# Optimization experiments

Measured on AMD Instinct MI355X. Metric: run time of the kernel, lower is better.

Reference implementation:

```python
import jax, jax.numpy as jnp
import numpy as np

K = 3
K2 = K * K
EPS = 1e-5


def conv2d(x, w, stride=1, pad=1):
    return jax.lax.conv_general_dilated(
        x, w, (stride, stride), [(pad, pad), (pad, pad)],
        dimension_numbers=("NCHW", "OIHW", "NCHW"))


def bilinear_sample(x, py, px):
    """x: [B,C,H,W]; py,px: [B,Ho,Wo,K2] float sample coords.
    Zero padding outside bounds (torchvision deform_conv2d semantics).
    Returns [B,C,Ho,Wo,K2]."""
    B, C, H, W = x.shape
    Ho, Wo = py.shape[1], py.shape[2]
    y0 = jnp.floor(py)
    x0 = jnp.floor(px)
    wy1 = py - y0
    wx1 = px - x0
    x_flat = x.reshape(B, C, H * W)

    def gather(yi, xi):
        valid = (yi >= 0) & (yi < H) & (xi >= 0) & (xi < W)
        yc = jnp.clip(yi, 0, H - 1).astype(jnp.int32)
        xc = jnp.clip(xi, 0, W - 1).astype(jnp.int32)
        idx = (yc * W + xc).reshape(B, 1, -1)          # [B,1,N]
        v = jnp.take_along_axis(x_flat, idx, axis=2)   # [B,C,N]
        return v * valid.reshape(B, 1, -1).astype(x.dtype)

    w00 = ((1 - wy1) * (1 - wx1)).reshape(B, 1, -1)
    w01 = ((1 - wy1) * wx1).reshape(B, 1, -1)
    w10 = (wy1 * (1 - wx1)).reshape(B, 1, -1)
    w11 = (wy1 * wx1).reshape(B, 1, -1)
    val = (w00 * gather(y0, x0) + w01 * gather(y0, x0 + 1)
           + w10 * gather(y0 + 1, x0) + w11 * gather(y0 + 1, x0 + 1))
    return val.reshape(B, C, Ho, Wo, K2)


def deform_conv_bn_relu(x, d, offset_w, conv_w, gamma, beta):
    # offset branch: 3x3 conv on d, clamp to [-1,1]
    offset = jnp.clip(conv2d(d, offset_w, 1, 1), -1.0, 1.0)  # [B,2*K2,H,W]
    B, Cin, H, W = x.shape
    Cout = conv_w.shape[0]
    off = offset.reshape(B, K2, 2, H, W)
    dy = off[:, :, 0].transpose(0, 2, 3, 1)  # [B,H,W,K2]
    dx = off[:, :, 1].transpose(0, 2, 3, 1)
    kh = (jnp.arange(K2) // K).astype(jnp.float32)
    kw = (jnp.arange(K2) % K).astype(jnp.float32)
    # sample coords: out pixel + kernel tap - padding + learned offset
    py = (jnp.arange(H, dtype=jnp.float32)[None, :, None, None] - 1.0
          + kh[None, None, None, :] + dy)
    px = (jnp.arange(W, dtype=jnp.float32)[None, None, :, None] - 1.0
          + kw[None, None, None, :] + dx)
    sampled = bilinear_sample(x, py, px)  # [B,Cin,H,W,K2]
    out = jnp.einsum('bchwk,ock->bohw', sampled,
                     conv_w.reshape(Cout, Cin, K2))
    # BatchNorm2d (training forward: biased batch stats) + ReLU
    mean = out.mean(axis=(0, 2, 3))
    var = out.var(axis=(0, 2, 3))
    inv = gamma / jnp.sqrt(var + EPS)
    out = (out - mean[None, :, None, None]) * inv[None, :, None, None] \
        + beta[None, :, None, None]
    out = jax.nn.relu(out)
    return out, offset


def setup_inputs() -> dict:
    key = jax.random.key(0)
    k1, k2, k3, k4 = jax.random.split(key, 4)
    B, C, H, W = 4, 64, 160, 160
    Cout, offC = 64, 64
    x = jax.random.normal(k1, (B, C, H, W), dtype=jnp.float32)
    d = jax.random.normal(k2, (B, offC, H, W), dtype=jnp.float32)
    # torch zero-inits offset_conv; use small random weights so the
    # bilinear gather path is actually exercised with fractional offsets
    offset_w = jax.random.normal(k3, (2 * K2, offC, K, K), dtype=jnp.float32) * 0.01
    conv_w = jax.random.normal(k4, (Cout, C, K, K), dtype=jnp.float32) * (1.0 / np.sqrt(C * K2))
    gamma = jnp.ones((Cout,), dtype=jnp.float32)
    beta = jnp.zeros((Cout,), dtype=jnp.float32)
    return {"x": x, "d": d, "offset_w": offset_w, "conv_w": conv_w,
            "gamma": gamma, "beta": beta}


def reference(x, d, offset_w, conv_w, gamma, beta):
    return deform_conv_bn_relu(x, d, offset_w, conv_w, gamma, beta)
```

## Files before the change

kernel.cpp:

```cpp
#include <hip/hip_runtime.h>
#include <hip/hip_bf16.h>

#define BB 4
#define HH 160
#define WW 160
#define HWD (HH * WW)
#define OUT_ELEMS (BB * 64 * HWD)
#define OFF_ELEMS (BB * 18 * HWD)
#define EPSBN 1e-5f
#define CHSTRIDE (8 * HWD)
#define NSLOT 256

typedef __attribute__((ext_vector_type(8))) short bf16x8;
typedef __attribute__((ext_vector_type(4))) float f32x4;

__device__ inline unsigned pack2bf(float a, float b) {
  __hip_bfloat162 h2 = __float22bfloat162_rn(float2{a, b});
  unsigned u;
  __builtin_memcpy(&u, &h2, 4);
  return u;
}
__device__ inline unsigned short bf16bits(float a) {
  __hip_bfloat16 h = __float2bfloat16(a);
  unsigned short u;
  __builtin_memcpy(&u, &h, 2);
  return u;
}

__device__ inline void tile_map(int blk, int& b, int& ty0, int& tx0) {
  int t = (blk & 7) * 200 + (blk >> 3);
  b = t / 400;
  int r = t % 400;
  ty0 = (r / 10) * 4;
  tx0 = (r % 10) * 16;
}

__global__ void prep_kernel(const float* __restrict__ cw,
                            const float* __restrict__ ow,
                            unsigned short* __restrict__ Bp,
                            unsigned short* __restrict__ B2p,
                            float* __restrict__ part) {
  int i = blockIdx.x * 256 + threadIdx.x;
  if (i < 32768) part[i] = 0.f;
  if (i < 49152) {
    int j = i & 7, l = (i >> 3) & 63, rest = i >> 9;
    int ki = rest % 24, nt = rest / 24;
    int kp = ki * 32 + ((l >> 4) << 3) + j;
    int chunk = kp / 96, kq = kp % 96;
    int t = kq >> 3, c = kq & 7;
    int n = nt * 16 + (l & 15);
    float v = (t < 9) ? cw[n * 576 + (chunk * 8 + c) * 9 + t] : 0.f;
    Bp[i] = bf16bits(v);
  }
  if (i < 24576) {
    int j = i & 7, l = (i >> 3) & 63, rest = i >> 9;
    int ki = rest % 24, nt = rest / 24;
    int kp = ki * 32 + ((l >> 4) << 3) + j;
    int chunk = kp / 96, kq = kp % 96;
    int t = kq >> 3, c = kq & 7;
    int n = nt * 16 + (l & 15);
    float v = (t < 9 && n < 18) ? ow[n * 576 + (chunk * 8 + c) * 9 + t] : 0.f;
    B2p[i] = bf16bits(v);
  }
}

__global__ __launch_bounds__(256) void offconv_kernel(
    const float* __restrict__ d, const bf16x8* __restrict__ B2p,
    float* __restrict__ off_out) {
  int b, ty0, tx0;
  tile_map(blockIdx.x, b, ty0, tx0);
  const int tid = threadIdx.x;
  const int wv = tid >> 6, lane = tid & 63;
  const int lo = lane >> 4, li = lane & 15;
  const int px = li, py = wv;

  __shared__ float p2[108 * 12];
  __shared__ bf16x8 Af[768];

  int poff[3];
  bool tre[3];
#pragma unroll
  for (int kk = 0; kk < 3; ++kk) {
    int t = kk * 4 + lo;
    tre[kk] = (t < 9);
    poff[kk] = tre[kk] ? ((py + t / 3) * 18 + px + t % 3) : 0;
  }

  int goff[4], laddr[4];
  bool gok[4];
#pragma unroll
  for (int i = 0; i < 4; ++i) {
    int l = tid + i * 256;
    int c = l / 108, rc = l % 108, r = rc / 18, col = rc % 18;
    int gy = ty0 - 1 + r, gx = tx0 - 1 + col;
    gok[i] = (l < 864) && gy >= 0 && gy < HH && gx >= 0 && gx < WW;
    goff[i] = ((b * 64 + c) * HH + gy) * WW + gx;
    laddr[i] = rc * 12 + c;
  }
  float g[4];
#pragma unroll
  for (int i = 0; i < 4; ++i) g[i] = gok[i] ? d[goff[i]] : 0.f;

  f32x4 acc0{0.f, 0.f, 0.f, 0.f}, acc1{0.f, 0.f, 0.f, 0.f};
  const int nt = wv >> 1, mh = wv & 1;

  for (int chunk = 0; chunk < 8; ++chunk) {
    bf16x8 bw0 = B2p[((nt * 24 + chunk * 3 + 0) << 6) + lane];
    bf16x8 bw1 = B2p[((nt * 24 + chunk * 3 + 1) << 6) + lane];
    bf16x8 bw2 = B2p[((nt * 24 + chunk * 3 + 2) << 6) + lane];
#pragma unroll
    for (int i = 0; i < 4; ++i) {
      int l = tid + i * 256;
      if (l < 864) p2[laddr[i]] = g[i];
    }
    __syncthreads();
    int nco = ((chunk < 7) ? (chunk + 1) : 7) * CHSTRIDE;
#pragma unroll
    for (int i = 0; i < 4; ++i) g[i] = gok[i] ? d[goff[i] + nco] : 0.f;
#pragma unroll
    for (int kk = 0; kk < 3; ++kk) {
      union { bf16x8 v; unsigned u[4]; } a;
      if (tre[kk]) {
        const float* q = p2 + poff[kk] * 12;
        float4 c0 = *(const float4*)(q);
        float4 c1 = *(const float4*)(q + 4);
        a.u[0] = pack2bf(c0.x, c0.y);
        a.u[1] = pack2bf(c0.z, c0.w);
        a.u[2] = pack2bf(c1.x, c1.y);
        a.u[3] = pack2bf(c1.z, c1.w);
      } else {
        a.u[0] = a.u[1] = a.u[2] = a.u[3] = 0u;
      }
      Af[((wv * 3 + kk) << 6) + lane] = a.v;
    }
    __syncthreads();
#pragma unroll
    for (int kk = 0; kk < 3; ++kk) {
      bf16x8 bw = (kk == 0) ? bw0 : (kk == 1) ? bw1 : bw2;
      acc0 = __builtin_amdgcn_mfma_f32_16x16x32_bf16(
          Af[(((mh * 2) * 3 + kk) << 6) + lane], bw, acc0, 0, 0, 0);
      acc1 = __builtin_amdgcn_mfma_f32_16x16x32_bf16(
          Af[(((mh * 2 + 1) * 3 + kk) << 6) + lane], bw, acc1, 0, 0, 0);
    }
  }
  const int n = nt * 16 + li;
  if (n < 18) {
#pragma unroll
    for (int f = 0; f < 2; ++f) {
      int mf = mh * 2 + f;
      f32x4 a = f ? acc1 : acc0;
      float* po = off_out + ((b * 18 + n) * HH + ty0 + mf) * WW + tx0 + lo * 4;
      float4 v;
      v.x = fminf(1.f, fmaxf(-1.f, a[0]));
      v.y = fminf(1.f, fmaxf(-1.f, a[1]));
      v.z = fminf(1.f, fmaxf(-1.f, a[2]));
      v.w = fminf(1.f, fmaxf(-1.f, a[3]));
      *(float4*)po = v;
    }
  }
}

__global__ __launch_bounds__(256) void dconv_kernel(
    const float* __restrict__ x, const float* __restrict__ offs,
    const bf16x8* __restrict__ Bp, float* __restrict__ out,
    float* __restrict__ part) {
  int b, ty0, tx0;
  tile_map(blockIdx.x, b, ty0, tx0);
  const int tid = threadIdx.x;
  const int wv = tid >> 6, lane = tid & 63;
  const int lo = lane >> 4, li = lane & 15;
  const int px = li, py = wv;
  const int h = ty0 + py, w = tx0 + px;

  __shared__ float patch[189 * 12];
  __shared__ bf16x8 Af[768];

  int bs[3];
  float W00[3], W01[3], W10[3], W11[3];
  bool tre[3];
#pragma unroll
  for (int kk = 0; kk < 3; ++kk) {
    int t = kk * 4 + lo;
    tre[kk] = (t < 9);
    if (tre[kk]) {
      float dy = offs[((b * 18 + 2 * t) * HH + h) * WW + w];
      float dx = offs[((b * 18 + 2 * t + 1) * HH + h) * WW + w];
      float pyf = (float)(h - 1 + t / 3) + dy;
      float pxf = (float)(w - 1 + t % 3) + dx;
      float y0 = floorf(pyf), x0 = floorf(pxf);
      float wy = pyf - y0, wx = pxf - x0;
      bs[kk] = ((int)y0 - (ty0 - 2)) * 21 + ((int)x0 - (tx0 - 2));
      W00[kk] = (1.f - wy) * (1.f - wx);
      W01[kk] = (1.f - wy) * wx;
      W10[kk] = wy * (1.f - wx);
      W11[kk] = wy * wx;
    } else {
      bs[kk] = 0;
      W00[kk] = W01[kk] = W10[kk] = W11[kk] = 0.f;
    }
  }

  int goff[6], laddr[6];
  bool gok[6];
#pragma unroll
  for (int i = 0; i < 6; ++i) {
    int l = tid + i * 256;
    int c = l / 189, rc = l % 189, r = rc / 21, col = rc % 21;
    int gy = ty0 - 2 + r, gx = tx0 - 2 + col;
    gok[i] = (l < 1512) && gy >= 0 && gy < HH && gx >= 0 && gx < WW;
    goff[i] = ((b * 64 + c) * HH + gy) * WW + gx;
    laddr[i] = rc * 12 + c;
  }
  float g[6];
#pragma unroll
  for (int i = 0; i < 6; ++i) g[i] = gok[i] ? x[goff[i]] : 0.f;

  f32x4 acc[4];
#pragma unroll
  for (int i = 0; i < 4; ++i) acc[i] = f32x4{0.f, 0.f, 0.f, 0.f};
  const int nt = wv;

  for (int chunk = 0; chunk < 8; ++chunk) {
    bf16x8 bw0 = Bp[((nt * 24 + chunk * 3 + 0) << 6) + lane];
    bf16x8 bw1 = Bp[((nt * 24 + chunk * 3 + 1) << 6) + lane];
    bf16x8 bw2 = Bp[((nt * 24 + chunk * 3 + 2) << 6) + lane];
#pragma unroll
    for (int i = 0; i < 6; ++i) {
      int l = tid + i * 256;
      if (l < 1512) patch[laddr[i]] = g[i];
    }
    __syncthreads();
    int nco = ((chunk < 7) ? (chunk + 1) : 7) * CHSTRIDE;
#pragma unroll
    for (int i = 0; i < 6; ++i) g[i] = gok[i] ? x[goff[i] + nco] : 0.f;
#pragma unroll
    for (int kk = 0; kk < 3; ++kk) {
      union { bf16x8 v; unsigned u[4]; } a;
      if (tre[kk]) {
        const float* q = patch + bs[kk] * 12;
        float4 p00a = *(const float4*)(q);
        float4 p00b = *(const float4*)(q + 4);
        float4 p01a = *(const float4*)(q + 12);
        float4 p01b = *(const float4*)(q + 16);
        float4 p10a = *(const float4*)(q + 252);
        float4 p10b = *(const float4*)(q + 256);
        float4 p11a = *(const float4*)(q + 264);
        float4 p11b = *(const float4*)(q + 268);
        float w0 = W00[kk], w1 = W01[kk], w2 = W10[kk], w3 = W11[kk];
        float v0 = fmaf(w3, p11a.x, fmaf(w2, p10a.x, fmaf(w1, p01a.x, w0 * p00a.x)));
        float v1 = fmaf(w3, p11a.y, fmaf(w2, p10a.y, fmaf(w1, p01a.y, w0 * p00a.y)));
        float v2 = fmaf(w3, p11a.z, fmaf(w2, p10a.z, fmaf(w1, p01a.z, w0 * p00a.z)));
        float v3 = fmaf(w3, p11a.w, fmaf(w2, p10a.w, fmaf(w1, p01a.w, w0 * p00a.w)));
        float v4 = fmaf(w3, p11b.x, fmaf(w2, p10b.x, fmaf(w1, p01b.x, w0 * p00b.x)));
        float v5 = fmaf(w3, p11b.y, fmaf(w2, p10b.y, fmaf(w1, p01b.y, w0 * p00b.y)));
        float v6 = fmaf(w3, p11b.z, fmaf(w2, p10b.z, fmaf(w1, p01b.z, w0 * p00b.z)));
        float v7 = fmaf(w3, p11b.w, fmaf(w2, p10b.w, fmaf(w1, p01b.w, w0 * p00b.w)));
        a.u[0] = pack2bf(v0, v1);
        a.u[1] = pack2bf(v2, v3);
        a.u[2] = pack2bf(v4, v5);
        a.u[3] = pack2bf(v6, v7);
      } else {
        a.u[0] = a.u[1] = a.u[2] = a.u[3] = 0u;
      }
      Af[((wv * 3 + kk) << 6) + lane] = a.v;
    }
    __syncthreads();
#pragma unroll
    for (int kk = 0; kk < 3; ++kk) {
      bf16x8 bw = (kk == 0) ? bw0 : (kk == 1) ? bw1 : bw2;
#pragma unroll
      for (int mf = 0; mf < 4; ++mf)
        acc[mf] = __builtin_amdgcn_mfma_f32_16x16x32_bf16(
            Af[((mf * 3 + kk) << 6) + lane], bw, acc[mf], 0, 0, 0);
    }
  }
  const int n = nt * 16 + li;
  float s = 0.f, s2 = 0.f;
#pragma unroll
  for (int mf = 0; mf < 4; ++mf) {
    float* po = out + ((b * 64 + n) * HH + ty0 + mf) * WW + tx0 + lo * 4;
    *(float4*)po = make_float4(acc[mf][0], acc[mf][1], acc[mf][2], acc[mf][3]);
#pragma unroll
    for (int r = 0; r < 4; ++r) {
      float v = acc[mf][r];
      s += v;
      s2 = fmaf(v, v, s2);
    }
  }
  s += __shfl_xor(s, 16);  s += __shfl_xor(s, 32);
  s2 += __shfl_xor(s2, 16); s2 += __shfl_xor(s2, 32);
  if (lo == 0) {
    int slot = blockIdx.x & (NSLOT - 1);
    atomicAdd(&part[n * NSLOT + slot], s);
    atomicAdd(&part[(64 + n) * NSLOT + slot], s2);
  }
}

__global__ __launch_bounds__(256) void reduce_kernel(
    const float* __restrict__ part, double* __restrict__ sums) {
  const int j = blockIdx.x;
  __shared__ double sh[256];
  sh[threadIdx.x] = (double)part[j * NSLOT + threadIdx.x];
  __syncthreads();
  for (int t = 128; t > 0; t >>= 1) {
    if (threadIdx.x < t) sh[threadIdx.x] += sh[threadIdx.x + t];
    __syncthreads();
  }
  if (threadIdx.x == 0) sums[j] = sh[0];
}

__global__ __launch_bounds__(256) void bnapply_kernel(
    float* __restrict__ out, const double* __restrict__ sums,
    const float* __restrict__ gamma, const float* __restrict__ beta) {
  const int i = blockIdx.x * 256 + threadIdx.x;
  if (i >= OUT_ELEMS / 4) return;
  const int o = (i / (HWD / 4)) & 63;
  const float n_inv = 1.0f / (float)(BB * HWD);
  float mean = (float)sums[o] * n_inv;
  float var = (float)sums[64 + o] * n_inv - mean * mean;
  float inv = gamma[o] * rsqrtf(var + EPSBN);
  float bt = beta[o];
  float4 v = ((float4*)out)[i];
  v.x = fmaxf(0.f, (v.x - mean) * inv + bt);
  v.y = fmaxf(0.f, (v.y - mean) * inv + bt);
  v.z = fmaxf(0.f, (v.z - mean) * inv + bt);
  v.w = fmaxf(0.f, (v.w - mean) * inv + bt);
  ((float4*)out)[i] = v;
}

extern "C" void kernel_launch(void* const* d_in, const int* in_sizes, int n_in,
                              void* d_out, int out_size, void* d_ws, size_t ws_size,
                              hipStream_t stream) {
  const float* x = (const float*)d_in[0];
  const float* d = (const float*)d_in[1];
  const float* ow = (const float*)d_in[2];
  const float* cw = (const float*)d_in[3];
  const float* gamma = (const float*)d_in[4];
  const float* beta = (const float*)d_in[5];

  float* out = (float*)d_out;
  float* off_out = out + OUT_ELEMS;

  double* sums = (double*)d_ws;
  unsigned short* Bp = (unsigned short*)((char*)d_ws + 1024);
  unsigned short* B2p = Bp + 49152;
  float* part = (float*)(B2p + 24576);

  prep_kernel<<<192, 256, 0, stream>>>(cw, ow, Bp, B2p, part);

  offconv_kernel<<<1600, 256, 0, stream>>>(d, (const bf16x8*)B2p, off_out);
  dconv_kernel<<<1600, 256, 0, stream>>>(x, off_out, (const bf16x8*)Bp, out,
                                         part);

  reduce_kernel<<<128, 256, 0, stream>>>(part, sums);
  bnapply_kernel<<<(OUT_ELEMS / 4 + 255) / 256, 256, 0, stream>>>(
      out, sums, gamma, beta);
}
```

Baseline: 166.9 us.

## Fuse offset conv and deformable conv into one kernel via shared-memory offsets

Merges the offset-convolution kernel into the deformable-convolution kernel so each tile computes its clamped offsets, stores them in shared memory, and reads them back directly instead of round-tripping through global memory. One kernel launch goes away, and the first x-patch loads are issued before the offset write-out so they overlap with it. The fused kernel needs more shared memory and registers, and it adds launch_bounds(256,4), which can push the compiler into register spills or limit occupancy.

```diff
diff --git a/kernel.cpp b/kernel.cpp
--- a/kernel.cpp
+++ b/kernel.cpp
@@ -64,105 +64,10 @@
   }
 }
 
-__global__ __launch_bounds__(256) void offconv_kernel(
-    const float* __restrict__ d, const bf16x8* __restrict__ B2p,
-    float* __restrict__ off_out) {
-  int b, ty0, tx0;
-  tile_map(blockIdx.x, b, ty0, tx0);
-  const int tid = threadIdx.x;
-  const int wv = tid >> 6, lane = tid & 63;
-  const int lo = lane >> 4, li = lane & 15;
-  const int px = li, py = wv;
-
-  __shared__ float p2[108 * 12];
-  __shared__ bf16x8 Af[768];
-
-  int poff[3];
-  bool tre[3];
-#pragma unroll
-  for (int kk = 0; kk < 3; ++kk) {
-    int t = kk * 4 + lo;
-    tre[kk] = (t < 9);
-    poff[kk] = tre[kk] ? ((py + t / 3) * 18 + px + t % 3) : 0;
-  }
-
-  int goff[4], laddr[4];
-  bool gok[4];
-#pragma unroll
-  for (int i = 0; i < 4; ++i) {
-    int l = tid + i * 256;
-    int c = l / 108, rc = l % 108, r = rc / 18, col = rc % 18;
-    int gy = ty0 - 1 + r, gx = tx0 - 1 + col;
-    gok[i] = (l < 864) && gy >= 0 && gy < HH && gx >= 0 && gx < WW;
-    goff[i] = ((b * 64 + c) * HH + gy) * WW + gx;
-    laddr[i] = rc * 12 + c;
-  }
-  float g[4];
-#pragma unroll
-  for (int i = 0; i < 4; ++i) g[i] = gok[i] ? d[goff[i]] : 0.f;
-
-  f32x4 acc0{0.f, 0.f, 0.f, 0.f}, acc1{0.f, 0.f, 0.f, 0.f};
-  const int nt = wv >> 1, mh = wv & 1;
-
-  for (int chunk = 0; chunk < 8; ++chunk) {
-    bf16x8 bw0 = B2p[((nt * 24 + chunk * 3 + 0) << 6) + lane];
-    bf16x8 bw1 = B2p[((nt * 24 + chunk * 3 + 1) << 6) + lane];
-    bf16x8 bw2 = B2p[((nt * 24 + chunk * 3 + 2) << 6) + lane];
-#pragma unroll
-    for (int i = 0; i < 4; ++i) {
-      int l = tid + i * 256;
-      if (l < 864) p2[laddr[i]] = g[i];
-    }
-    __syncthreads();
-    int nco = ((chunk < 7) ? (chunk + 1) : 7) * CHSTRIDE;
-#pragma unroll
-    for (int i = 0; i < 4; ++i) g[i] = gok[i] ? d[goff[i] + nco] : 0.f;
-#pragma unroll
-    for (int kk = 0; kk < 3; ++kk) {
-      union { bf16x8 v; unsigned u[4]; } a;
-      if (tre[kk]) {
-        const float* q = p2 + poff[kk] * 12;
-        float4 c0 = *(const float4*)(q);
-        float4 c1 = *(const float4*)(q + 4);
-        a.u[0] = pack2bf(c0.x, c0.y);
-        a.u[1] = pack2bf(c0.z, c0.w);
-        a.u[2] = pack2bf(c1.x, c1.y);
-        a.u[3] = pack2bf(c1.z, c1.w);
-      } else {
-        a.u[0] = a.u[1] = a.u[2] = a.u[3] = 0u;
-      }
-      Af[((wv * 3 + kk) << 6) + lane] = a.v;
-    }
-    __syncthreads();
-#pragma unroll
-    for (int kk = 0; kk < 3; ++kk) {
-      bf16x8 bw = (kk == 0) ? bw0 : (kk == 1) ? bw1 : bw2;
-      acc0 = __builtin_amdgcn_mfma_f32_16x16x32_bf16(
-          Af[(((mh * 2) * 3 + kk) << 6) + lane], bw, acc0, 0, 0, 0);
-      acc1 = __builtin_amdgcn_mfma_f32_16x16x32_bf16(
-          Af[(((mh * 2 + 1) * 3 + kk) << 6) + lane], bw, acc1, 0, 0, 0);
-    }
-  }
-  const int n = nt * 16 + li;
-  if (n < 18) {
-#pragma unroll
-    for (int f = 0; f < 2; ++f) {
-      int mf = mh * 2 + f;
-      f32x4 a = f ? acc1 : acc0;
-      float* po = off_out + ((b * 18 + n) * HH + ty0 + mf) * WW + tx0 + lo * 4;
-      float4 v;
-      v.x = fminf(1.f, fmaxf(-1.f, a[0]));
-      v.y = fminf(1.f, fmaxf(-1.f, a[1]));
-      v.z = fminf(1.f, fmaxf(-1.f, a[2]));
-      v.w = fminf(1.f, fmaxf(-1.f, a[3]));
-      *(float4*)po = v;
-    }
-  }
-}
-
-__global__ __launch_bounds__(256) void dconv_kernel(
-    const float* __restrict__ x, const float* __restrict__ offs,
-    const bf16x8* __restrict__ Bp, float* __restrict__ out,
+__global__ __launch_bounds__(256, 4) void fused_kernel(
+    const float* __restrict__ x, const float* __restrict__ d,
+    const bf16x8* __restrict__ Bp, const bf16x8* __restrict__ B2p,
+    float* __restrict__ out, float* __restrict__ off_out,
     float* __restrict__ part) {
   int b, ty0, tx0;
   tile_map(blockIdx.x, b, ty0, tx0);
@@ -174,6 +79,116 @@
 
   __shared__ float patch[189 * 12];
   __shared__ bf16x8 Af[768];
+  __shared__ float offs_s[64 * 18];
+
+  int goffx[6], laddrx[6];
+  bool gokx[6];
+#pragma unroll
+  for (int i = 0; i < 6; ++i) {
+    int l = tid + i * 256;
+    int c = l / 189, rc = l % 189, r = rc / 21, col = rc % 21;
+    int gy = ty0 - 2 + r, gx = tx0 - 2 + col;
+    gokx[i] = (l < 1512) && gy >= 0 && gy < HH && gx >= 0 && gx < WW;
+    goffx[i] = ((b * 64 + c) * HH + gy) * WW + gx;
+    laddrx[i] = rc * 12 + c;
+  }
+
+  f32x4 acc0{0.f, 0.f, 0.f, 0.f}, acc1{0.f, 0.f, 0.f, 0.f};
+  const int ntA = wv >> 1, mh = wv & 1;
+  {
+    int poff[3];
+    bool tre[3];
+#pragma unroll
+    for (int kk = 0; kk < 3; ++kk) {
+      int t = kk * 4 + lo;
+      tre[kk] = (t < 9);
+      poff[kk] = tre[kk] ? ((py + t / 3) * 18 + px + t % 3) : 0;
+    }
+
+    int goff[4], laddr[4];
+    bool gok[4];
+#pragma unroll
+    for (int i = 0; i < 4; ++i) {
+      int l = tid + i * 256;
+      int c = l / 108, rc = l % 108, r = rc / 18, col = rc % 18;
+      int gy = ty0 - 1 + r, gx = tx0 - 1 + col;
+      gok[i] = (l < 864) && gy >= 0 && gy < HH && gx < WW && gx >= 0;
+      goff[i] = ((b * 64 + c) * HH + gy) * WW + gx;
+      laddr[i] = rc * 12 + c;
+    }
+    float g[4];
+#pragma unroll
+    for (int i = 0; i < 4; ++i) g[i] = gok[i] ? d[goff[i]] : 0.f;
+
+    for (int chunk = 0; chunk < 8; ++chunk) {
+      bf16x8 bw0 = B2p[((ntA * 24 + chunk * 3 + 0) << 6) + lane];
+      bf16x8 bw1 = B2p[((ntA * 24 + chunk * 3 + 1) << 6) + lane];
+      bf16x8 bw2 = B2p[((ntA * 24 + chunk * 3 + 2) << 6) + lane];
+#pragma unroll
+      for (int i = 0; i < 4; ++i) {
+        int l = tid + i * 256;
+        if (l < 864) patch[laddr[i]] = g[i];
+      }
+      __syncthreads();
+      int nco = ((chunk < 7) ? (chunk + 1) : 7) * CHSTRIDE;
+#pragma unroll
+      for (int i = 0; i < 4; ++i) g[i] = gok[i] ? d[goff[i] + nco] : 0.f;
+#pragma unroll
+      for (int kk = 0; kk < 3; ++kk) {
+        union { bf16x8 v; unsigned u[4]; } a;
+        if (tre[kk]) {
+          const float* q = patch + poff[kk] * 12;
+          float4 c0 = *(const float4*)(q);
+          float4 c1 = *(const float4*)(q + 4);
+          a.u[0] = pack2bf(c0.x, c0.y);
+          a.u[1] = pack2bf(c0.z, c0.w);
+          a.u[2] = pack2bf(c1.x, c1.y);
+          a.u[3] = pack2bf(c1.z, c1.w);
+        } else {
+          a.u[0] = a.u[1] = a.u[2] = a.u[3] = 0u;
+        }
+        Af[((wv * 3 + kk) << 6) + lane] = a.v;
+      }
+      __syncthreads();
+#pragma unroll
+      for (int kk = 0; kk < 3; ++kk) {
+        bf16x8 bw = (kk == 0) ? bw0 : (kk == 1) ? bw1 : bw2;
+        acc0 = __builtin_amdgcn_mfma_f32_16x16x32_bf16(
+            Af[(((mh * 2) * 3 + kk) << 6) + lane], bw, acc0, 0, 0, 0);
+        acc1 = __builtin_amdgcn_mfma_f32_16x16x32_bf16(
+            Af[(((mh * 2 + 1) * 3 + kk) << 6) + lane], bw, acc1, 0, 0, 0);
+      }
+    }
+  }
+
+  float gv[6];
+#pragma unroll
+  for (int i = 0; i < 6; ++i) gv[i] = gokx[i] ? x[goffx[i]] : 0.f;
+
+  {
+    const int n = ntA * 16 + li;
+    if (n < 18) {
+#pragma unroll
+      for (int f = 0; f < 2; ++f) {
+        int mf = mh * 2 + f;
+        f32x4 a = f ? acc1 : acc0;
+        float* po =
+            off_out + ((b * 18 + n) * HH + ty0 + mf) * WW + tx0 + lo * 4;
+        float4 v;
+        v.x = fminf(1.f, fmaxf(-1.f, a[0]));
+        v.y = fminf(1.f, fmaxf(-1.f, a[1]));
+        v.z = fminf(1.f, fmaxf(-1.f, a[2]));
+        v.w = fminf(1.f, fmaxf(-1.f, a[3]));
+        *(float4*)po = v;
+        int pix = mf * 16 + lo * 4;
+        offs_s[(pix + 0) * 18 + n] = v.x;
+        offs_s[(pix + 1) * 18 + n] = v.y;
+        offs_s[(pix + 2) * 18 + n] = v.z;
+        offs_s[(pix + 3) * 18 + n] = v.w;
+      }
+    }
+  }
+  __syncthreads();
 
   int bs[3];
   float W00[3], W01[3], W10[3], W11[3];
@@ -183,8 +198,8 @@
     int t = kk * 4 + lo;
     tre[kk] = (t < 9);
     if (tre[kk]) {
-      float dy = offs[((b * 18 + 2 * t) * HH + h) * WW + w];
-      float dx = offs[((b * 18 + 2 * t + 1) * HH + h) * WW + w];
+      float dy = offs_s[(py * 16 + px) * 18 + 2 * t];
+      float dx = offs_s[(py * 16 + px) * 18 + 2 * t + 1];
       float pyf = (float)(h - 1 + t / 3) + dy;
       float pxf = (float)(w - 1 + t % 3) + dx;
       float y0 = floorf(pyf), x0 = floorf(pxf);
@@ -200,21 +215,6 @@
     }
   }
 
-  int goff[6], laddr[6];
-  bool gok[6];
-#pragma unroll
-  for (int i = 0; i < 6; ++i) {
-    int l = tid + i * 256;
-    int c = l / 189, rc = l % 189, r = rc / 21, col = rc % 21;
-    int gy = ty0 - 2 + r, gx = tx0 - 2 + col;
-    gok[i] = (l < 1512) && gy >= 0 && gy < HH && gx >= 0 && gx < WW;
-    goff[i] = ((b * 64 + c) * HH + gy) * WW + gx;
-    laddr[i] = rc * 12 + c;
-  }
-  float g[6];
-#pragma unroll
-  for (int i = 0; i < 6; ++i) g[i] = gok[i] ? x[goff[i]] : 0.f;
-
   f32x4 acc[4];
 #pragma unroll
   for (int i = 0; i < 4; ++i) acc[i] = f32x4{0.f, 0.f, 0.f, 0.f};
@@ -227,12 +227,12 @@
 #pragma unroll
     for (int i = 0; i < 6; ++i) {
       int l = tid + i * 256;
-      if (l < 1512) patch[laddr[i]] = g[i];
+      if (l < 1512) patch[laddrx[i]] = gv[i];
     }
     __syncthreads();
     int nco = ((chunk < 7) ? (chunk + 1) : 7) * CHSTRIDE;
 #pragma unroll
-    for (int i = 0; i < 6; ++i) g[i] = gok[i] ? x[goff[i] + nco] : 0.f;
+    for (int i = 0; i < 6; ++i) gv[i] = gokx[i] ? x[goffx[i] + nco] : 0.f;
 #pragma unroll
     for (int kk = 0; kk < 3; ++kk) {
       union { bf16x8 v; unsigned u[4]; } a;
@@ -348,8 +348,8 @@
 
   prep_kernel<<<192, 256, 0, stream>>>(cw, ow, Bp, B2p, part);
 
-  offconv_kernel<<<1600, 256, 0, stream>>>(d, (const bf16x8*)B2p, off_out);
-  dconv_kernel<<<1600, 256, 0, stream>>>(x, off_out, (const bf16x8*)Bp, out,
+  fused_kernel<<<1600, 256, 0, stream>>>(x, d, (const bf16x8*)Bp,
+                                         (const bf16x8*)B2p, out, off_out,
                                          part);
 
   reduce_kernel<<<128, 256, 0, stream>>>(part, sums);
```

After: 161.7 us. 3.1% less time.
